# Optimization experiments

Measured on AMD Instinct MI355X. Metric: run time of the kernel, lower is better.

Reference implementation:

```python
import jax, jax.numpy as jnp
import numpy as np

SPATIAL_SCALE = 0.25
N, C, H, W = 8, 256, 128, 128
P = 100000
IMG = 512.0  # image-space extent (H / spatial_scale)


def setup_inputs() -> dict:
    key = jax.random.key(0)
    k1, k2, k3, k4 = jax.random.split(key, 4)
    features = jax.random.normal(k1, (N, C, H, W), dtype=jnp.float32)
    batch_idx = jax.random.randint(k2, (P,), 0, N).astype(jnp.float32)
    xy = jax.random.uniform(k3, (P, 2), dtype=jnp.float32) * IMG
    rois = jnp.concatenate([batch_idx[:, None], xy], axis=1)  # [P,3]: (b, x, y)
    return {"features": features, "rois": rois}


def _interp(features, rois, spatial_scale):
    n, c, h, w = features.shape
    b = rois[:, 0].astype(jnp.int32)
    x = rois[:, 1] * spatial_scale
    y = rois[:, 2] * spatial_scale
    # RoIAlign-style bilinear interpolation with boundary handling
    valid = (y >= -1.0) & (y <= h) & (x >= -1.0) & (x <= w)
    y = jnp.maximum(y, 0.0)
    x = jnp.maximum(x, 0.0)
    y_low = jnp.floor(y).astype(jnp.int32)
    x_low = jnp.floor(x).astype(jnp.int32)
    y_at_edge = y_low >= h - 1
    x_at_edge = x_low >= w - 1
    y_low = jnp.minimum(y_low, h - 1)
    x_low = jnp.minimum(x_low, w - 1)
    y_high = jnp.where(y_at_edge, y_low, y_low + 1)
    x_high = jnp.where(x_at_edge, x_low, x_low + 1)
    y = jnp.where(y_at_edge, y_low.astype(y.dtype), y)
    x = jnp.where(x_at_edge, x_low.astype(x.dtype), x)
    ly = y - y_low
    lx = x - x_low
    hy = 1.0 - ly
    hx = 1.0 - lx
    w1 = (hy * hx)[:, None]  # [P,1]
    w2 = (hy * lx)[:, None]
    w3 = (ly * hx)[:, None]
    w4 = (ly * lx)[:, None]
    # fancy-index gather: [P, C] per corner
    v1 = features[b, :, y_low, x_low]
    v2 = features[b, :, y_low, x_high]
    v3 = features[b, :, y_high, x_low]
    v4 = features[b, :, y_high, x_high]
    out = w1 * v1 + w2 * v2 + w3 * v3 + w4 * v4  # [P, C]
    return jnp.where(valid[:, None], out, 0.0)


def reference(features, rois):
    return _interp(features, rois, SPATIAL_SCALE)
```

## Files before the change

kernel.cpp:

```cpp
#include <hip/hip_runtime.h>

#define SCALE   0.25f
#define NBATCH  8
#define CCH     256
#define HH      128
#define WW      128
#define NBUCK   (NBATCH * HH)
#define CG      16
#define NCG     (CCH / CG)
#define CAP     160
#define PADC    257


__device__ __forceinline__ int bucket_of(const float* __restrict__ rois, int p) {
    int b = (int)rois[3 * p];
    float y = rois[3 * p + 2] * SCALE;
    y = fmaxf(y, 0.0f);
    int yl = (int)floorf(y);
    yl = min(yl, HH - 1);
    return b * HH + yl;
}

__global__ void k_zero(int* cnt) {
    cnt[blockIdx.x * 256 + threadIdx.x] = 0;
}

__global__ void k_bin(const float* __restrict__ rois, int* cnt, int* slots, int P) {
    int p = blockIdx.x * 256 + threadIdx.x;
    if (p < P) {
        int bk = bucket_of(rois, p);
        int pos = atomicAdd(&cnt[bk], 1);
        if (pos < CAP) slots[bk * CAP + pos] = p;
    }
}

__global__ __launch_bounds__(256, 8) void k_main(
    const float* __restrict__ feat, const float* __restrict__ rois,
    const int* __restrict__ slots, const int* __restrict__ cnt_arr,
    float* __restrict__ out)
{
    const int bk = blockIdx.x >> 4;
    const int cg = blockIdx.x & 15;
    const int cnt = min(cnt_arr[bk], CAP);
    if (cnt == 0) return;
    const int b  = bk >> 7;
    const int yl = bk & 127;
    const int yh = min(yl + 1, HH - 1);

    __shared__ float lds[CG * PADC];

    const int t = threadIdx.x;
    const float* base = feat + (size_t)(b * CCH + cg * CG) * (HH * WW);
#pragma unroll
    for (int k = 0; k < 4; ++k) {
        int id  = k * 256 + t;
        int x4  = id & 31;
        int row = (id >> 5) & 1;
        int c   = id >> 6;
        int y   = row ? yh : yl;
        float4 v = *(const float4*)(base + (size_t)c * (HH * WW) + y * WW + x4 * 4);
        float* d = &lds[c * PADC + row * WW + x4];
        d[0]  = v.x;
        d[32] = v.y;
        d[64] = v.z;
        d[96] = v.w;
    }
    __syncthreads();

    const int wv   = t >> 6;
    const int lane = t & 63;
    const int c    = lane & 15;
    const int sub  = lane >> 4;
    const float* ldc = &lds[c * PADC];
    const int sbase = bk * CAP;

    for (int ii = wv * 4; ii < cnt; ii += 16) {
        int i = ii + sub;
        bool act = (i < cnt);
        int p = slots[sbase + (act ? i : 0)];
        float x = rois[3 * p + 1] * SCALE;
        float y = rois[3 * p + 2] * SCALE;
        bool valid = (y >= -1.0f) && (y <= (float)HH) &&
                     (x >= -1.0f) && (x <= (float)WW);
        y = fmaxf(y, 0.0f);
        x = fmaxf(x, 0.0f);

        int ylo = (int)floorf(y);
        float yf = y;
        if (ylo >= HH - 1) { ylo = HH - 1; yf = (float)ylo; }
        int xlo = (int)floorf(x);
        float xf = x;
        int xhi;
        if (xlo >= WW - 1) { xlo = WW - 1; xhi = WW - 1; xf = (float)xlo; }
        else               { xhi = xlo + 1; }

        float ly = yf - (float)ylo;
        float lx = xf - (float)xlo;
        float hy = 1.0f - ly, hx = 1.0f - lx;
        float w1 = hy * hx, w2 = hy * lx, w3 = ly * hx, w4 = ly * lx;
        if (!valid) { w1 = 0.0f; w2 = 0.0f; w3 = 0.0f; w4 = 0.0f; }

        int flo = ((xlo & 3) << 5) + (xlo >> 2);
        int fhi = ((xhi & 3) << 5) + (xhi >> 2);
        float v1 = ldc[flo];
        float v2 = ldc[fhi];
        float v3 = ldc[WW + flo];
        float v4 = ldc[WW + fhi];
        float r = w1 * v1 + w2 * v2 + w3 * v3 + w4 * v4;
        if (act) out[(size_t)p * CCH + cg * CG + c] = r;
    }
}

extern "C" void kernel_launch(void* const* d_in, const int* in_sizes, int n_in,
                              void* d_out, int out_size, void* d_ws, size_t ws_size,
                              hipStream_t stream) {
    const float* feat = (const float*)d_in[0];
    const float* rois = (const float*)d_in[1];
    float* out = (float*)d_out;
    const int P = in_sizes[1] / 3;

    int* cnt   = (int*)d_ws;
    int* slots = cnt + NBUCK;

    const int pb = (P + 255) / 256;
    k_zero<<<NBUCK / 256, 256, 0, stream>>>(cnt);
    k_bin<<<pb, 256, 0, stream>>>(rois, cnt, slots, P);
    k_main<<<NBUCK * NCG, 256, 0, stream>>>(feat, rois, slots, cnt, out);
}
```

Baseline: 277.7 us.

## Precompute interpolation params in binning pass and process two channels per thread

The binning kernel now computes per-point LDS offsets, validity and fractional weights once and stores them as an int4 slot record. The main kernel then reads that record instead of re-reading rois and redoing the index maths in each of the 16 channel-group blocks. Each thread handles two adjacent channels and writes them with a float2 store, and the zeroing kernel is replaced by hipMemsetAsync. The trade-off is four times more slot storage and write traffic in the binning pass.

```diff
diff --git a/kernel.cpp b/kernel.cpp
--- a/kernel.cpp
+++ b/kernel.cpp
@@ -12,32 +12,40 @@
 #define PADC    257
 
 
-__device__ __forceinline__ int bucket_of(const float* __restrict__ rois, int p) {
-    int b = (int)rois[3 * p];
-    float y = rois[3 * p + 2] * SCALE;
-    y = fmaxf(y, 0.0f);
-    int yl = (int)floorf(y);
-    yl = min(yl, HH - 1);
-    return b * HH + yl;
-}
-
-__global__ void k_zero(int* cnt) {
-    cnt[blockIdx.x * 256 + threadIdx.x] = 0;
-}
-
-__global__ void k_bin(const float* __restrict__ rois, int* cnt, int* slots, int P) {
+__global__ void k_bin(const float* __restrict__ rois, int* __restrict__ cnt,
+                      int4* __restrict__ slots, int P) {
     int p = blockIdx.x * 256 + threadIdx.x;
-    if (p < P) {
-        int bk = bucket_of(rois, p);
-        int pos = atomicAdd(&cnt[bk], 1);
-        if (pos < CAP) slots[bk * CAP + pos] = p;
-    }
+    if (p >= P) return;
+    float fb = rois[3 * p];
+    float fx = rois[3 * p + 1] * SCALE;
+    float fy = rois[3 * p + 2] * SCALE;
+    int b = (int)fb;
+    bool valid = (fy >= -1.0f) && (fy <= (float)HH) &&
+                 (fx >= -1.0f) && (fx <= (float)WW);
+    float y = fmaxf(fy, 0.0f);
+    float x = fmaxf(fx, 0.0f);
+    int ylo = (int)floorf(y);
+    int xlo = (int)floorf(x);
+    float yf = y, xf = x;
+    int xhi;
+    if (ylo >= HH - 1) { ylo = HH - 1; yf = (float)ylo; }
+    if (xlo >= WW - 1) { xlo = WW - 1; xhi = WW - 1; xf = (float)xlo; }
+    else               { xhi = xlo + 1; }
+    float ly = yf - (float)ylo;
+    float lx = xf - (float)xlo;
+    int flo = ((xlo & 3) << 5) | (xlo >> 2);
+    int fhi = ((xhi & 3) << 5) | (xhi >> 2);
+    unsigned pk = (unsigned)flo | ((unsigned)fhi << 8) | (valid ? 0u : 0x80000000u);
+    int bk = b * HH + ylo;
+    int pos = atomicAdd(&cnt[bk], 1);
+    if (pos < CAP)
+        slots[bk * CAP + pos] =
+            make_int4(p, (int)pk, __float_as_int(lx), __float_as_int(ly));
 }
 
 __global__ __launch_bounds__(256, 8) void k_main(
-    const float* __restrict__ feat, const float* __restrict__ rois,
-    const int* __restrict__ slots, const int* __restrict__ cnt_arr,
-    float* __restrict__ out)
+    const float* __restrict__ feat, const int4* __restrict__ slots,
+    const int* __restrict__ cnt_arr, float* __restrict__ out)
 {
     const int bk = blockIdx.x >> 4;
     const int cg = blockIdx.x & 15;
@@ -69,45 +77,35 @@
 
     const int wv   = t >> 6;
     const int lane = t & 63;
-    const int c    = lane & 15;
-    const int sub  = lane >> 4;
-    const float* ldc = &lds[c * PADC];
-    const int sbase = bk * CAP;
+    const int sub  = lane >> 3;
+    const int c0   = (lane & 7) << 1;
+    const float* ldc = &lds[c0 * PADC];
+    const int4* sb = slots + bk * CAP;
 
-    for (int ii = wv * 4; ii < cnt; ii += 16) {
+    for (int ii = wv * 8; ii < cnt; ii += 32) {
         int i = ii + sub;
         bool act = (i < cnt);
-        int p = slots[sbase + (act ? i : 0)];
-        float x = rois[3 * p + 1] * SCALE;
-        float y = rois[3 * p + 2] * SCALE;
-        bool valid = (y >= -1.0f) && (y <= (float)HH) &&
-                     (x >= -1.0f) && (x <= (float)WW);
-        y = fmaxf(y, 0.0f);
-        x = fmaxf(x, 0.0f);
+        int4 r = sb[act ? i : cnt - 1];
+        unsigned pk = (unsigned)r.y;
+        float lx = __int_as_float(r.z);
+        float ly = __int_as_float(r.w);
+        float s  = ((int)pk < 0) ? 0.0f : 1.0f;
+        float hy = (1.0f - ly) * s;
+        float lys = ly * s;
+        float hx = 1.0f - lx;
+        float w1 = hy * hx, w2 = hy * lx, w3 = lys * hx, w4 = lys * lx;
+        int flo = pk & 255;
+        int fhi = (pk >> 8) & 255;
 
-        int ylo = (int)floorf(y);
-        float yf = y;
-        if (ylo >= HH - 1) { ylo = HH - 1; yf = (float)ylo; }
-        int xlo = (int)floorf(x);
-        float xf = x;
-        int xhi;
-        if (xlo >= WW - 1) { xlo = WW - 1; xhi = WW - 1; xf = (float)xlo; }
-        else               { xhi = xlo + 1; }
+        float v1 = ldc[flo], v2 = ldc[fhi];
+        float v3 = ldc[WW + flo], v4 = ldc[WW + fhi];
+        float o0 = w1 * v1 + w2 * v2 + w3 * v3 + w4 * v4;
+        v1 = ldc[PADC + flo]; v2 = ldc[PADC + fhi];
+        v3 = ldc[PADC + WW + flo]; v4 = ldc[PADC + WW + fhi];
+        float o1 = w1 * v1 + w2 * v2 + w3 * v3 + w4 * v4;
 
-        float ly = yf - (float)ylo;
-        float lx = xf - (float)xlo;
-        float hy = 1.0f - ly, hx = 1.0f - lx;
-        float w1 = hy * hx, w2 = hy * lx, w3 = ly * hx, w4 = ly * lx;
-        if (!valid) { w1 = 0.0f; w2 = 0.0f; w3 = 0.0f; w4 = 0.0f; }
-
-        int flo = ((xlo & 3) << 5) + (xlo >> 2);
-        int fhi = ((xhi & 3) << 5) + (xhi >> 2);
-        float v1 = ldc[flo];
-        float v2 = ldc[fhi];
-        float v3 = ldc[WW + flo];
-        float v4 = ldc[WW + fhi];
-        float r = w1 * v1 + w2 * v2 + w3 * v3 + w4 * v4;
-        if (act) out[(size_t)p * CCH + cg * CG + c] = r;
+        if (act)
+            *(float2*)(out + (size_t)r.x * CCH + cg * CG + c0) = make_float2(o0, o1);
     }
 }
 
@@ -119,11 +117,11 @@
     float* out = (float*)d_out;
     const int P = in_sizes[1] / 3;
 
-    int* cnt   = (int*)d_ws;
-    int* slots = cnt + NBUCK;
+    int*  cnt   = (int*)d_ws;
+    int4* slots = (int4*)((char*)d_ws + NBUCK * sizeof(int));
 
+    hipMemsetAsync(cnt, 0, NBUCK * sizeof(int), stream);
     const int pb = (P + 255) / 256;
-    k_zero<<<NBUCK / 256, 256, 0, stream>>>(cnt);
     k_bin<<<pb, 256, 0, stream>>>(rois, cnt, slots, P);
-    k_main<<<NBUCK * NCG, 256, 0, stream>>>(feat, rois, slots, cnt, out);
+    k_main<<<NBUCK * NCG, 256, 0, stream>>>(feat, slots, cnt, out);
 }
```

After: 266.2 us. -4.2%, faster.
